# Performance work log

Hardware: AMD Instinct MI355X
Metric: run time of the kernel (lower is better)

The kernel has to match this reference:

```python
import jax, jax.numpy as jnp
import numpy as np

N_NODES = 100000
N_GRAPHS = 256


def gcn_conv(x, W, b, src, dst, n_nodes):
    # PyG GCNConv: h = x @ W; out_i = sum_{(j->i)} norm_e * h_j + norm_ii * h_i + b
    # with self-loops added and norm = deg^{-1/2}[src] * deg^{-1/2}[dst],
    # deg counting self-loops.
    h = x @ W                                            # [N, H]
    ones = jnp.ones(src.shape[0], dtype=x.dtype)
    deg = jax.ops.segment_sum(ones, dst, num_segments=n_nodes) + 1.0  # +1 self-loop
    dis = jax.lax.rsqrt(deg)                             # deg >= 1 always
    norm = dis[src] * dis[dst]                           # [E]
    msg = h[src] * norm[:, None]                         # [E, H] gather + scale
    agg = jax.ops.segment_sum(msg, dst, num_segments=n_nodes)         # scatter-add
    self_loop = h * (dis * dis)[:, None]                 # norm_ii = dis_i^2
    return agg + self_loop + b


def setup_inputs() -> dict:
    key = jax.random.key(0)
    ks = jax.random.split(key, 8)
    C_IN, H = 64, 64
    E = 1600000
    x = jax.random.normal(ks[0], (N_NODES, C_IN), dtype=jnp.float32)
    edge_index = jax.random.randint(ks[1], (2, E), 0, N_NODES, dtype=jnp.int64)
    batch = jnp.sort(jax.random.randint(ks[2], (N_NODES,), 0, N_GRAPHS, dtype=jnp.int64))
    s = 0.1
    W1 = jax.random.normal(ks[3], (C_IN, H), dtype=jnp.float32) * s
    W2 = jax.random.normal(ks[4], (H, H), dtype=jnp.float32) * s
    W3 = jax.random.normal(ks[5], (H, H), dtype=jnp.float32) * s
    Wl = jax.random.normal(ks[6], (H, 1), dtype=jnp.float32) * s
    b1 = jnp.zeros((H,), jnp.float32)
    b2 = jnp.zeros((H,), jnp.float32)
    b3 = jnp.zeros((H,), jnp.float32)
    bl = jnp.zeros((1,), jnp.float32)
    return {"x": x, "edge_index": edge_index, "batch": batch,
            "W1": W1, "b1": b1, "W2": W2, "b2": b2, "W3": W3, "b3": b3,
            "Wl": Wl, "bl": bl}


def reference(x, edge_index, batch, W1, b1, W2, b2, W3, b3, Wl, bl):
    src, dst = edge_index[0], edge_index[1]
    n = x.shape[0]
    h = jax.nn.relu(gcn_conv(x, W1, b1, src, dst, n))
    h = jax.nn.relu(gcn_conv(h, W2, b2, src, dst, n))
    h = gcn_conv(h, W3, b3, src, dst, n)
    # global_mean_pool over graph ids
    sums = jax.ops.segment_sum(h, batch, num_segments=N_GRAPHS)        # [G, H]
    cnt = jax.ops.segment_sum(jnp.ones((n,), h.dtype), batch, num_segments=N_GRAPHS)
    pooled = sums / jnp.maximum(cnt, 1.0)[:, None]
    # dropout p=0.5 is identity at inference (training=False)
    return pooled @ Wl + bl                                            # [G, 1]
```

## Files before the change

kernel.cpp:

```cpp
#include <hip/hip_runtime.h>

#define NGRAPHS 256
#define GBUCKET 256
#define CAP 8192
#define BUCKET_BLOCKS 512
#define MAXE 16

typedef unsigned long long u64;
typedef unsigned int u32;


__global__ __launch_bounds__(256) void k_bucket(const int* __restrict__ src,
                                                const int* __restrict__ dst,
                                                int E, int N,
                                                int* __restrict__ bcur,
                                                u32* __restrict__ bpair) {
    __shared__ int hist[GBUCKET], base[GBUCKET], cur[GBUCKET];
    int t = threadIdx.x;
    int chunk = (E + gridDim.x - 1) / gridDim.x;
    int s0 = blockIdx.x * chunk;
    int s1 = s0 + chunk; if (s1 > E) s1 = E;
    if (s0 >= E) return;
    for (int i = t; i < GBUCKET; i += 256) hist[i] = 0;
    __syncthreads();

    u32 pcache[MAXE]; int bcache[MAXE];
#pragma unroll
    for (int u = 0; u < MAXE; ++u) {
        int e = s0 + t + u * 256;
        bool ok = e < s1;
        int d = ok ? __builtin_nontemporal_load(&dst[e]) : 0;
        int s = ok ? __builtin_nontemporal_load(&src[e]) : 0;
        int bkt = (int)(((long long)d * GBUCKET) / N);
        int lo  = (int)(((long long)bkt * N + GBUCKET - 1) / GBUCKET);
        pcache[u] = ((u32)(d - lo) << 17) | (u32)s;
        bcache[u] = ok ? bkt : -1;
        if (ok) atomicAdd(&hist[bkt], 1);
    }
    __syncthreads();
    for (int i = t; i < GBUCKET; i += 256) {
        base[i] = atomicAdd(&bcur[i], hist[i]);
        cur[i] = 0;
    }
    __syncthreads();
#pragma unroll
    for (int u = 0; u < MAXE; ++u) {
        int bkt = bcache[u];
        if (bkt >= 0) {
            int off = atomicAdd(&cur[bkt], 1);
            __builtin_nontemporal_store(pcache[u], &bpair[(size_t)bkt * CAP + base[bkt] + off]);
        }
    }
}


__global__ __launch_bounds__(512) void k_csr(const int* __restrict__ bcur,
                                             const u32* __restrict__ bpair,
                                             int N, int E,
                                             int* __restrict__ row_start,
                                             float* __restrict__ dis,
                                             int* __restrict__ csr_src) {
    __shared__ u32 pe[CAP];
    __shared__ int cnts[512];
    __shared__ int scanbuf[512];
    __shared__ int cursors[512];
    __shared__ int bb[GBUCKET];
    __shared__ int bbase_s, bcnt_s;
    int g = blockIdx.x;
    int t = threadIdx.x;

    for (int i = t; i < GBUCKET; i += 512) bb[i] = bcur[i];
    cnts[t] = 0;
    __syncthreads();
    if (t == 0) {
        int s = 0;
        for (int k = 0; k < g; ++k) s += bb[k];
        bbase_s = s;
        bcnt_s = bb[g];
    }
    __syncthreads();
    int bbase = bbase_s;
    int cnt   = bcnt_s;

    int lo = (int)(((long long)g * N + GBUCKET - 1) / GBUCKET);
    int hi = (int)(((long long)(g + 1) * N + GBUCKET - 1) / GBUCKET);
    int nn = hi - lo;

    const u32* bp = bpair + (size_t)g * CAP;
    for (int i = t; i < cnt; i += 512) {
        u32 p = __builtin_nontemporal_load(&bp[i]);
        pe[i] = p;
        atomicAdd(&cnts[p >> 17], 1);
    }
    __syncthreads();

    int v = cnts[t];
    scanbuf[t] = v;
    __syncthreads();
    for (int o = 1; o < 512; o <<= 1) {
        int add = (t >= o) ? scanbuf[t - o] : 0;
        __syncthreads();
        scanbuf[t] += add;
        __syncthreads();
    }
    int excl = scanbuf[t] - v;

    if (t < nn) {
        row_start[lo + t] = bbase + excl;
        dis[lo + t] = rsqrtf((float)v + 1.0f);
    }
    if (g == GBUCKET - 1 && t == 0) row_start[N] = E;
    cursors[t] = excl;
    __syncthreads();

    for (int i = t; i < cnt; i += 512) {
        u32 p = pe[i];
        int dloc = p >> 17;
        int s = (int)(p & 0x1FFFFu);
        int pos = bbase + atomicAdd(&cursors[dloc], 1);
        csr_src[pos] = s;
    }
}


__global__ __launch_bounds__(256) void k_gemm_reg(const float* __restrict__ X,
                                                  const float* __restrict__ W,
                                                  const float* __restrict__ dis,
                                                  float* __restrict__ G, int N) {
    int lane = threadIdx.x & 63;
    int wid = (blockIdx.x * blockDim.x + threadIdx.x) >> 6;
    int nw = (gridDim.x * blockDim.x) >> 6;

    float wreg[64];
#pragma unroll
    for (int k = 0; k < 64; ++k) wreg[k] = W[k * 64 + lane];

    for (int r = wid; r < N; r += nw) {
        int ru = __builtin_amdgcn_readfirstlane(r);
        const float* xr = X + (size_t)ru * 64;
        float a0 = 0.f, a1 = 0.f, a2 = 0.f, a3 = 0.f;
#pragma unroll
        for (int k = 0; k < 64; k += 4) {
            a0 = fmaf(xr[k + 0], wreg[k + 0], a0);
            a1 = fmaf(xr[k + 1], wreg[k + 1], a1);
            a2 = fmaf(xr[k + 2], wreg[k + 2], a2);
            a3 = fmaf(xr[k + 3], wreg[k + 3], a3);
        }
        float a = (a0 + a1) + (a2 + a3);
        G[(size_t)ru * 64 + lane] = a * dis[ru];
    }
}


template <bool RELU, bool POOL>
__global__ __launch_bounds__(256) void k_agg(const float* __restrict__ g,
                                             const float* __restrict__ dis,
                                             const int* __restrict__ row_start,
                                             const int* __restrict__ csr_src,
                                             const float* __restrict__ b,
                                             float* __restrict__ out, int N,
                                             const float* __restrict__ Wl,
                                             float* __restrict__ hdot) {
    int wave0 = (blockIdx.x * blockDim.x + threadIdx.x) >> 6;
    int nwaves = (gridDim.x * blockDim.x) >> 6;
    int lane = threadIdx.x & 63;
    int sub  = lane >> 4;
    int q    = lane & 15;
    const float4* g4 = (const float4*)g;

    for (int wid = wave0; wid < N; wid += nwaves) {
        int beg = row_start[wid];
        int end = row_start[wid + 1];

        float4 acc;
        if (sub == 0) acc = g4[(size_t)wid * 16 + q];
        else          acc = make_float4(0.f, 0.f, 0.f, 0.f);

        int e = beg;
        for (; e + 8 <= end; e += 8) {
            int sA = csr_src[e + sub];
            int sB = csr_src[e + 4 + sub];
            float4 a = g4[(size_t)sA * 16 + q];
            float4 c = g4[(size_t)sB * 16 + q];
            acc.x += a.x; acc.y += a.y; acc.z += a.z; acc.w += a.w;
            acc.x += c.x; acc.y += c.y; acc.z += c.z; acc.w += c.w;
        }
        if (e + 4 <= end) {
            int sA = csr_src[e + sub];
            float4 a = g4[(size_t)sA * 16 + q];
            acc.x += a.x; acc.y += a.y; acc.z += a.z; acc.w += a.w;
            e += 4;
        }
        int rem = end - e;
        if (sub < rem) {
            int sA = csr_src[e + sub];
            float4 a = g4[(size_t)sA * 16 + q];
            acc.x += a.x; acc.y += a.y; acc.z += a.z; acc.w += a.w;
        }

#pragma unroll
        for (int o = 16; o <= 32; o <<= 1) {
            acc.x += __shfl_xor(acc.x, o);
            acc.y += __shfl_xor(acc.y, o);
            acc.z += __shfl_xor(acc.z, o);
            acc.w += __shfl_xor(acc.w, o);
        }

        if (sub == 0) {
            float d = dis[wid];
            float4 bv = ((const float4*)b)[q];
            float4 v;
            v.x = fmaf(acc.x, d, bv.x);
            v.y = fmaf(acc.y, d, bv.y);
            v.z = fmaf(acc.z, d, bv.z);
            v.w = fmaf(acc.w, d, bv.w);
            if (RELU) {
                v.x = fmaxf(v.x, 0.f); v.y = fmaxf(v.y, 0.f);
                v.z = fmaxf(v.z, 0.f); v.w = fmaxf(v.w, 0.f);
            }
            if (POOL) {
                float4 wl = ((const float4*)Wl)[q];
                float s = v.x * wl.x + v.y * wl.y + v.z * wl.z + v.w * wl.w;
                s += __shfl_xor(s, 1);
                s += __shfl_xor(s, 2);
                s += __shfl_xor(s, 4);
                s += __shfl_xor(s, 8);
                if (q == 0) hdot[wid] = s;
            } else {
                ((float4*)out)[(size_t)wid * 16 + q] = v;
            }
        }
    }
}


__global__ __launch_bounds__(256) void k_poolfin(const float* __restrict__ hdot,
                                                 const int* __restrict__ batch,
                                                 const float* __restrict__ bl,
                                                 float* __restrict__ out, int N) {
    int g = blockIdx.x;
    int lo = 0, hi = N;
    while (lo < hi) { int m = (lo + hi) >> 1; if (batch[m] < g) lo = m + 1; else hi = m; }
    int start = lo;
    hi = N;
    while (lo < hi) { int m = (lo + hi) >> 1; if (batch[m] <= g) lo = m + 1; else hi = m; }
    int end = lo;

    float part = 0.0f;
    for (int i = start + threadIdx.x; i < end; i += 256)
        part += hdot[i];
    for (int o = 32; o; o >>= 1) part += __shfl_down(part, o);
    __shared__ float ps[4];
    int lane = threadIdx.x & 63;
    int wv = threadIdx.x >> 6;
    if (lane == 0) ps[wv] = part;
    __syncthreads();
    if (threadIdx.x == 0) {
        float s = ps[0] + ps[1] + ps[2] + ps[3];
        float cnt = (float)(end - start);
        out[g] = s / fmaxf(cnt, 1.0f) + bl[0];
    }
}


extern "C" void kernel_launch(void* const* d_in, const int* in_sizes, int n_in,
                              void* d_out, int out_size, void* d_ws, size_t ws_size,
                              hipStream_t stream) {
    const float* x     = (const float*)d_in[0];
    const int*   ei    = (const int*)d_in[1];
    const int*   batch = (const int*)d_in[2];
    const float* W1 = (const float*)d_in[3];
    const float* b1 = (const float*)d_in[4];
    const float* W2 = (const float*)d_in[5];
    const float* b2 = (const float*)d_in[6];
    const float* W3 = (const float*)d_in[7];
    const float* b3 = (const float*)d_in[8];
    const float* Wl = (const float*)d_in[9];
    const float* bl = (const float*)d_in[10];
    float* out = (float*)d_out;

    const int N = in_sizes[0] / 64;
    const int E = in_sizes[1] / 2;
    const int* src = ei;
    const int* dst = ei + E;

    char* w = (char*)d_ws;
    auto alloc = [&](size_t bytes) -> void* {
        void* p = (void*)w;
        w += (bytes + 255) & ~(size_t)255;
        return p;
    };
    float* hA        = (float*)alloc((size_t)N * 64 * 4);
    float* hB        = (float*)alloc((size_t)N * 64 * 4);
    int*   csr       = (int*)alloc((size_t)E * 4);
    float* dis       = (float*)alloc((size_t)N * 4);
    int*   row_start = (int*)alloc((size_t)(N + 1) * 4);
    int*   bcur      = (int*)alloc((size_t)GBUCKET * 4);
    float* hdot      = (float*)alloc((size_t)N * 4);

    u32* bpair = (u32*)hA;

    (void)hipMemsetAsync(bcur, 0, (size_t)GBUCKET * 4, stream);

    k_bucket<<<BUCKET_BLOCKS, 256, 0, stream>>>(src, dst, E, N, bcur, bpair);
    k_csr<<<GBUCKET, 512, 0, stream>>>(bcur, bpair, N, E, row_start, dis, csr);

    int gmb = 2048;
    int ab = 2048;

    k_gemm_reg<<<gmb, 256, 0, stream>>>(x, W1, dis, hA, N);
    k_agg<true, false><<<ab, 256, 0, stream>>>(hA, dis, row_start, csr, b1, hB, N, Wl, nullptr);
    k_gemm_reg<<<gmb, 256, 0, stream>>>(hB, W2, dis, hA, N);
    k_agg<true, false><<<ab, 256, 0, stream>>>(hA, dis, row_start, csr, b2, hB, N, Wl, nullptr);
    k_gemm_reg<<<gmb, 256, 0, stream>>>(hB, W3, dis, hA, N);
    k_agg<false, true><<<ab, 256, 0, stream>>>(hA, dis, row_start, csr, b3, nullptr, N, Wl, hdot);

    k_poolfin<<<NGRAPHS, 256, 0, stream>>>(hdot, batch, bl, out, N);
}
```

Measured before the change: 358.7 us.

## Split aggregation feature dimension into two halves across interleaved blocks

The aggregation kernel now splits each node's 64-wide feature row into two 32-float halves, each handled by a separate block group. Within a wave, 8 lanes cover a half-row and 8 edge slots run in parallel, so each wave processes more edges per iteration. Block ids are interleaved so the two halves of the same node range run on neighbouring blocks. The pooled dot product is written as two partial arrays and summed in the final pooling kernel. This doubles the CSR index reads and node loop overhead in exchange for more edge-level parallelism and a smaller gathered footprint per wave.

```diff
diff --git a/kernel.cpp b/kernel.cpp
--- a/kernel.cpp
+++ b/kernel.cpp
@@ -161,54 +161,60 @@
                                              float* __restrict__ out, int N,
                                              const float* __restrict__ Wl,
                                              float* __restrict__ hdot) {
-    int wave0 = (blockIdx.x * blockDim.x + threadIdx.x) >> 6;
-    int nwaves = (gridDim.x * blockDim.x) >> 6;
+    int bid = blockIdx.x;
+    int half = (bid >> 2) & 1;
+    int idx  = ((bid >> 3) << 2) + (bid & 3);
+    int wv   = threadIdx.x >> 6;
     int lane = threadIdx.x & 63;
-    int sub  = lane >> 4;
-    int q    = lane & 15;
+    int slot = lane >> 3;
+    int c    = lane & 7;
+    int hc   = half * 8 + c;
+
+    int wave0 = idx * 4 + wv;
+    int nw = (gridDim.x >> 1) * 4;
     const float4* g4 = (const float4*)g;
 
-    for (int wid = wave0; wid < N; wid += nwaves) {
+    for (int wid = wave0; wid < N; wid += nw) {
         int beg = row_start[wid];
         int end = row_start[wid + 1];
 
         float4 acc;
-        if (sub == 0) acc = g4[(size_t)wid * 16 + q];
-        else          acc = make_float4(0.f, 0.f, 0.f, 0.f);
+        if (slot == 0) acc = g4[(size_t)wid * 16 + hc];
+        else           acc = make_float4(0.f, 0.f, 0.f, 0.f);
 
         int e = beg;
-        for (; e + 8 <= end; e += 8) {
-            int sA = csr_src[e + sub];
-            int sB = csr_src[e + 4 + sub];
-            float4 a = g4[(size_t)sA * 16 + q];
-            float4 c = g4[(size_t)sB * 16 + q];
+        for (; e + 16 <= end; e += 16) {
+            int sA = csr_src[e + slot];
+            int sB = csr_src[e + 8 + slot];
+            float4 a = g4[(size_t)sA * 16 + hc];
+            float4 d2 = g4[(size_t)sB * 16 + hc];
             acc.x += a.x; acc.y += a.y; acc.z += a.z; acc.w += a.w;
-            acc.x += c.x; acc.y += c.y; acc.z += c.z; acc.w += c.w;
-        }
-        if (e + 4 <= end) {
-            int sA = csr_src[e + sub];
-            float4 a = g4[(size_t)sA * 16 + q];
+            acc.x += d2.x; acc.y += d2.y; acc.z += d2.z; acc.w += d2.w;
+        }
+        if (e + 8 <= end) {
+            int sA = csr_src[e + slot];
+            float4 a = g4[(size_t)sA * 16 + hc];
             acc.x += a.x; acc.y += a.y; acc.z += a.z; acc.w += a.w;
-            e += 4;
+            e += 8;
         }
         int rem = end - e;
-        if (sub < rem) {
-            int sA = csr_src[e + sub];
-            float4 a = g4[(size_t)sA * 16 + q];
+        if (slot < rem) {
+            int sA = csr_src[e + slot];
+            float4 a = g4[(size_t)sA * 16 + hc];
             acc.x += a.x; acc.y += a.y; acc.z += a.z; acc.w += a.w;
         }
 
 #pragma unroll
-        for (int o = 16; o <= 32; o <<= 1) {
+        for (int o = 8; o <= 32; o <<= 1) {
             acc.x += __shfl_xor(acc.x, o);
             acc.y += __shfl_xor(acc.y, o);
             acc.z += __shfl_xor(acc.z, o);
             acc.w += __shfl_xor(acc.w, o);
         }
 
-        if (sub == 0) {
+        if (slot == 0) {
             float d = dis[wid];
-            float4 bv = ((const float4*)b)[q];
+            float4 bv = ((const float4*)b)[hc];
             float4 v;
             v.x = fmaf(acc.x, d, bv.x);
             v.y = fmaf(acc.y, d, bv.y);
@@ -219,15 +225,14 @@
                 v.z = fmaxf(v.z, 0.f); v.w = fmaxf(v.w, 0.f);
             }
             if (POOL) {
-                float4 wl = ((const float4*)Wl)[q];
+                float4 wl = ((const float4*)Wl)[hc];
                 float s = v.x * wl.x + v.y * wl.y + v.z * wl.z + v.w * wl.w;
                 s += __shfl_xor(s, 1);
                 s += __shfl_xor(s, 2);
                 s += __shfl_xor(s, 4);
-                s += __shfl_xor(s, 8);
-                if (q == 0) hdot[wid] = s;
+                if (c == 0) hdot[(size_t)half * N + wid] = s;
             } else {
-                ((float4*)out)[(size_t)wid * 16 + q] = v;
+                ((float4*)out)[(size_t)wid * 16 + hc] = v;
             }
         }
     }
@@ -248,7 +253,7 @@
 
     float part = 0.0f;
     for (int i = start + threadIdx.x; i < end; i += 256)
-        part += hdot[i];
+        part += hdot[i] + hdot[(size_t)N + i];
     for (int o = 32; o; o >>= 1) part += __shfl_down(part, o);
     __shared__ float ps[4];
     int lane = threadIdx.x & 63;
@@ -296,7 +301,7 @@
     float* dis       = (float*)alloc((size_t)N * 4);
     int*   row_start = (int*)alloc((size_t)(N + 1) * 4);
     int*   bcur      = (int*)alloc((size_t)GBUCKET * 4);
-    float* hdot      = (float*)alloc((size_t)N * 4);
+    float* hdot      = (float*)alloc((size_t)N * 2 * 4);
 
     u32* bpair = (u32*)hA;
 
```

Result: slower. 369.3 us (+3.0%).
